# Kernel tuning notes

Hardware: AMD Instinct MI355X
Metric: run time of the kernel (lower is better)

Reference implementation:

```python
import jax, jax.numpy as jnp
import numpy as np

B = 65536
N_HOSTS = 16
N_FEATS = 48        # 3 * n_hosts
N_WINDOW = 3
N_LATENT = 10
GAT_IN = 3
GAT_OUT = 16
E = N_WINDOW + GAT_OUT  # 19, MHA embed dim
PROTO_DIM = 10


def setup_inputs() -> dict:
    key = jax.random.key(0)
    ks = jax.random.split(key, 20)
    def rn(k, shape, scale=0.1):
        return jax.random.normal(k, shape, dtype=jnp.float32) * scale
    return {
        "t": jax.random.normal(ks[0], (B, N_WINDOW, N_FEATS), dtype=jnp.float32),
        "s": jnp.zeros((1,), jnp.float32),  # unused by forward, kept for signature fidelity
        "h0": jax.random.normal(ks[1], (B, 1, N_WINDOW), dtype=jnp.float32),
        "gru_Wih": rn(ks[2], (3 * N_WINDOW, N_FEATS)),
        "gru_Whh": rn(ks[3], (3 * N_WINDOW, N_WINDOW)),
        "gru_bih": rn(ks[4], (3 * N_WINDOW,)),
        "gru_bhh": rn(ks[5], (3 * N_WINDOW,)),
        "gat_W": rn(ks[6], (GAT_IN, GAT_OUT)),
        "gat_al": rn(ks[7], (GAT_OUT,)),
        "gat_ar": rn(ks[8], (GAT_OUT,)),
        "mha_Win": rn(ks[9], (3 * E, E)),
        "mha_bin": rn(ks[10], (3 * E,)),
        "mha_Wout": rn(ks[11], (E, E)),
        "mha_bout": rn(ks[12], (E,)),
        "enc_W": rn(ks[13], (N_HOSTS * N_LATENT, N_WINDOW * E)),
        "enc_b": rn(ks[14], (N_HOSTS * N_LATENT,)),
        "anom_W": rn(ks[15], (2, N_LATENT)),
        "anom_b": rn(ks[16], (2,)),
        "proto_W": rn(ks[17], (PROTO_DIM, N_LATENT)),
        "proto_b": rn(ks[18], (PROTO_DIM,)),
    }


def _forward(t, s, h0, gru_Wih, gru_Whh, gru_bih, gru_bhh,
             gat_W, gat_al, gat_ar, mha_Win, mha_bin, mha_Wout, mha_bout,
             enc_W, enc_b, anom_W, anom_b, proto_W, proto_b):
    # ---- GRU (seq-first, batch B, hidden = n_window = 3) ----
    xs = jnp.swapaxes(t, 0, 1)  # (3, B, 48)
    h0_ = h0[:, 0, :]           # (B, 3)

    def gru_step(h, x_t):
        gi = x_t @ gru_Wih.T + gru_bih   # (B, 9)
        gh = h @ gru_Whh.T + gru_bhh     # (B, 9)
        i_r, i_z, i_n = jnp.split(gi, 3, axis=-1)
        h_r, h_z, h_n = jnp.split(gh, 3, axis=-1)
        r = jax.nn.sigmoid(i_r + h_r)
        z = jax.nn.sigmoid(i_z + h_z)
        n = jnp.tanh(i_n + r * h_n)
        h_new = (1.0 - z) * n + z * h
        return h_new, h_new

    _, gru_out = jax.lax.scan(gru_step, h0_, xs)  # (3, B, 3)

    # ---- GAT on fully-connected 16-node graph (with self loops) ----
    gin = t.reshape(t.shape[0], N_WINDOW, N_HOSTS, GAT_IN)      # (B, 3, 16, 3)
    z = jnp.einsum("bwnc,cf->bwnf", gin, gat_W)                 # (B, 3, 16, 16)
    el = z @ gat_al                                              # src scores (B,3,16)
    er = z @ gat_ar                                              # dst scores (B,3,16)
    e = jax.nn.leaky_relu(er[..., :, None] + el[..., None, :], 0.2)  # (B,3,v,u)
    alpha = jax.nn.softmax(e, axis=-1)                           # softmax over sources u
    gat_nodes = jnp.einsum("bwvu,bwuf->bwvf", alpha, z)          # (B, 3, 16, 16)
    gat_out = gat_nodes.mean(axis=2)                             # (B, 3, 16) mean over hosts
    gat_out = jnp.swapaxes(gat_out, 0, 1)                        # (3, B, 16)

    # ---- concat + single-head MHA (embed=19) ----
    c = jnp.concatenate([gru_out, gat_out], axis=-1)             # (3, B, 19)
    Wq, Wk, Wv = jnp.split(mha_Win, 3, axis=0)
    bq, bk, bv = jnp.split(mha_bin, 3, axis=0)
    q = c @ Wq.T + bq
    k = c @ Wk.T + bk
    v = c @ Wv.T + bv
    scores = jnp.einsum("sbe,tbe->bst", q, k) / jnp.sqrt(jnp.float32(E))
    attw = jax.nn.softmax(scores, axis=-1)
    attn = jnp.einsum("bst,tbe->sbe", attw, v)
    attn = attn @ mha_Wout.T + mha_bout                          # (3, B, 19)

    # ---- encoder: Linear(57,160); LeakyReLU(True) => negative_slope=1.0 => identity ----
    flat = jnp.swapaxes(attn, 0, 1).reshape(-1, N_WINDOW * E)    # (B, 57), seq-major flatten
    latent = flat @ enc_W.T + enc_b                              # (B, 160)
    latent = latent.reshape(-1, N_HOSTS, N_LATENT)               # (B, 16, 10)

    # ---- per-host tiny decoders, vectorized ----
    anomaly = jax.nn.softmax(latent @ anom_W.T + anom_b, axis=-1)   # (B, 16, 2)
    proto = jax.nn.sigmoid(latent @ proto_W.T + proto_b)            # (B, 16, PROTO_DIM)
    return anomaly, proto


def reference(t, s, h0, gru_Wih, gru_Whh, gru_bih, gru_bhh,
              gat_W, gat_al, gat_ar, mha_Win, mha_bin, mha_Wout, mha_bout,
              enc_W, enc_b, anom_W, anom_b, proto_W, proto_b):
    return _forward(t, s, h0, gru_Wih, gru_Whh, gru_bih, gru_bhh,
                    gat_W, gat_al, gat_ar, mha_Win, mha_bin, mha_Wout, mha_bout,
                    enc_W, enc_b, anom_W, anom_b, proto_W, proto_b)
```

## Files before the change

### kernel.cpp

```cpp
#include <hip/hip_runtime.h>

#define NW 3
#define NF 48
#define NHOST 16
#define NLAT 10
#define GOUT 16
#define EDIM 19
#define PDIM 10

#define CB_M    0
#define CB_P    361
#define CB_G    722
#define CB_H    741
#define CB_R    760
#define CB_C0   779
#define CB_WAL  780
#define CB_WAR  783
#define CB_CBIG 800
#define CB_BF   976
#define CB_TOT  10240

typedef __attribute__((ext_vector_type(8))) short bf16x8;
typedef __attribute__((ext_vector_type(4))) float f32x4;

__device__ __forceinline__ float frcp(float x){ return __builtin_amdgcn_rcpf(x); }
__device__ __forceinline__ float fsig(float x){ return frcp(1.f + __expf(-x)); }
__device__ __forceinline__ float ftanh(float x){ return 1.f - 2.f*frcp(1.f + __expf(2.f*x)); }
__device__ __forceinline__ unsigned short f2bf(float x){
    union { float f; unsigned u; } v; v.f = x;
    unsigned r = v.u + 0x7FFFu + ((v.u >> 16) & 1u);
    return (unsigned short)(r >> 16);
}
__device__ __forceinline__ float bf2f(unsigned short s){
    union { unsigned u; float f; } v; v.u = ((unsigned)s) << 16; return v.f;
}

__global__ __launch_bounds__(256) void k_const(
    const float* __restrict__ Win, const float* __restrict__ bin,
    const float* __restrict__ Wout, const float* __restrict__ bout,
    const float* __restrict__ gatW, const float* __restrict__ gal,
    const float* __restrict__ gar, const float* __restrict__ encW,
    const float* __restrict__ encb,
    const float* __restrict__ aW, const float* __restrict__ ab,
    const float* __restrict__ pW, const float* __restrict__ pb,
    float* __restrict__ cb)
{
    const int w = blockIdx.x*blockDim.x + threadIdx.x;
    if (w < 786) {
        const int idx = w;
        float acc = 0.f;
        if (idx < 361) {
            int i = idx/19, j = idx%19;
            for (int e = 0; e < EDIM; ++e) acc += Win[e*EDIM+i]*Win[(EDIM+e)*EDIM+j];
        } else if (idx < 722) {
            int k = idx-361; int i = k/19, j = k%19;
            for (int e = 0; e < EDIM; ++e) acc += Wout[i*EDIM+e]*Win[(2*EDIM+e)*EDIM+j];
        } else if (idx < 741) {
            int j = idx-722;
            for (int e = 0; e < EDIM; ++e) acc += bin[e]*Win[(EDIM+e)*EDIM+j];
        } else if (idx < 760) {
            int i = idx-741;
            for (int e = 0; e < EDIM; ++e) acc += Win[e*EDIM+i]*bin[EDIM+e];
        } else if (idx < 779) {
            int i = idx-760; acc = bout[i];
            for (int e = 0; e < EDIM; ++e) acc += Wout[i*EDIM+e]*bin[2*EDIM+e];
        } else if (idx == 779) {
            for (int e = 0; e < EDIM; ++e) acc += bin[e]*bin[EDIM+e];
        } else {
            int c = idx-780; int cc = c%3; bool left = c<3;
            for (int f2 = 0; f2 < GOUT; ++f2)
                acc += gatW[cc*GOUT+f2]*(left ? gal[f2] : gar[f2]);
        }
        cb[idx] = acc;
    } else if (w < 962) {
        const int g = w - 786;
        int host = g / 11, jj = g % 11;
        float acc = (jj == 0) ? (ab[0] - ab[1]) : pb[jj-1];
        for (int l = 0; l < NLAT; ++l) {
            float coef = (jj == 0) ? (aW[l] - aW[NLAT+l]) : pW[(jj-1)*NLAT + l];
            acc += coef * encb[host*NLAT + l];
        }
        cb[CB_CBIG + g] = acc;
    } else if (w < 12226) {
        unsigned short* bf = (unsigned short*)(cb + CB_BF);
        const int u = w - 962;
        int j    = u & 7;
        int lane = (u >> 3) & 63;
        int tile = u >> 9;
        int half = tile / 11, n = tile % 11;
        int k = half*32 + ((lane >> 4) & 3)*8 + j;
        int g = n*16 + (lane & 15);
        float acc = 0.f;
        if (k < 57) {
            int host = g / 11, jj = g % 11;
            for (int l = 0; l < NLAT; ++l) {
                float coef = (jj == 0) ? (aW[l] - aW[NLAT+l]) : pW[(jj-1)*NLAT + l];
                acc += coef * encW[(host*NLAT + l)*57 + k];
            }
        }
        bf[u] = f2bf(acc);
    }
}

__global__ __launch_bounds__(64, 4) void k_fused(
    const float* __restrict__ t, const float* __restrict__ h0,
    const float* __restrict__ Wih, const float* __restrict__ bih,
    const float* __restrict__ gatW, const float* __restrict__ Whh,
    const float* __restrict__ bhh, const float* __restrict__ cb,
    float* __restrict__ outA, float* __restrict__ outP, int B)
{
    __shared__ __align__(16) char smraw[9600];
    __shared__ __align__(16) unsigned short a2[16][64];
    float (*fm)[25][16]     = reinterpret_cast<float(*)[25][16]>(smraw);
    unsigned short (*xs)[50]= reinterpret_cast<unsigned short(*)[50]>(smraw + 4800);
    float (*mtb)[EDIM][16]  = reinterpret_cast<float(*)[EDIM][16]>(smraw + 4800);
    float (*pcb)[EDIM][16]  = reinterpret_cast<float(*)[EDIM][16]>(smraw + 4800);
    float (*gtb)[16]        = reinterpret_cast<float(*)[16]>(smraw + 4800 + 3648);
    _Float16 (*lg)[178]     = reinterpret_cast<_Float16(*)[178]>(smraw);

    const int lane = threadIdx.x;
    const int b0   = blockIdx.x * 16;
    const int bl   = lane & 15;
    const int sw   = lane >> 4;

    if (lane < 48) {
        const int w = sw;
        const float* tp = t + ((size_t)(b0 + bl)*NW + w)*NF;
        unsigned short* xrow = xs[lane];

        const float Wal0=cb[CB_WAL],Wal1=cb[CB_WAL+1],Wal2=cb[CB_WAL+2];
        const float War0=cb[CB_WAR],War1=cb[CB_WAR+1],War2=cb[CB_WAR+2];

        float gi[9];
#pragma unroll
        for (int r = 0; r < 9; ++r) gi[r] = bih[r];
        float el[NHOST], er[NHOST];
#pragma unroll
        for (int c = 0; c < 4; ++c) {
            float xc[12];
#pragma unroll
            for (int i = 0; i < 3; ++i) {
                float4 v = *reinterpret_cast<const float4*>(tp + c*12 + i*4);
                xc[i*4+0]=v.x; xc[i*4+1]=v.y; xc[i*4+2]=v.z; xc[i*4+3]=v.w;
            }
#pragma unroll
            for (int k = 0; k < 12; ++k) xrow[c*12 + k] = f2bf(xc[k]);
#pragma unroll
            for (int r = 0; r < 9; ++r) {
                float a = 0.f;
#pragma unroll
                for (int k = 0; k < 12; ++k) a += xc[k]*Wih[r*NF + c*12 + k];
                gi[r] += a;
            }
#pragma unroll
            for (int u = 0; u < 4; ++u) {
                const int uu = c*4 + u;
                el[uu] = xc[u*3]*Wal0 + xc[u*3+1]*Wal1 + xc[u*3+2]*Wal2;
                er[uu] = xc[u*3]*War0 + xc[u*3+1]*War1 + xc[u*3+2]*War2;
            }
        }
#pragma unroll
        for (int r = 0; r < 9; ++r) fm[w][r][bl] = gi[r];

        float beta[NHOST];
#pragma unroll
        for (int u = 0; u < NHOST; ++u) beta[u] = 0.f;
#pragma unroll
        for (int v = 0; v < NHOST; ++v) {
            float ee[NHOST]; float sum = 0.f;
#pragma unroll
            for (int u = 0; u < NHOST; ++u) {
                float s = er[v] + el[u];
                s = fmaxf(s, 0.2f*s);
                ee[u] = __expf(s); sum += ee[u];
            }
            float inv = frcp(sum);
#pragma unroll
            for (int u = 0; u < NHOST; ++u) beta[u] += ee[u]*inv;
        }
        float g0=0.f, g1=0.f, g2=0.f;
#pragma unroll
        for (int u = 0; u < NHOST; ++u) {
            float bu = beta[u]*(1.f/16.f);
            g0 += bu*bf2f(xrow[u*3+0]);
            g1 += bu*bf2f(xrow[u*3+1]);
            g2 += bu*bf2f(xrow[u*3+2]);
        }
#pragma unroll
        for (int f2 = 0; f2 < GOUT; ++f2)
            fm[w][9+f2][bl] = g0*gatW[f2] + g1*gatW[GOUT+f2] + g2*gatW[2*GOUT+f2];
    }
    __syncthreads();

    float cw[EDIM];
    float hsv = 0.f, aw0 = 0.f, aw1 = 0.f, aw2 = 0.f;
#pragma unroll
    for (int i = 0; i < EDIM; ++i) cw[i] = 0.f;

    if (lane < 48) {
        const int s = sw;
        const int b = b0 + bl;
        float h[3] = { h0[(size_t)b*3+0], h0[(size_t)b*3+1], h0[(size_t)b*3+2] };
        float ch[NW][3];
#pragma unroll
        for (int w = 0; w < NW; ++w) {
            float gi[9];
#pragma unroll
            for (int r = 0; r < 9; ++r) gi[r] = fm[w][r][bl];
            float gh[9];
#pragma unroll
            for (int r = 0; r < 9; ++r)
                gh[r] = bhh[r] + h[0]*Whh[r*3+0] + h[1]*Whh[r*3+1] + h[2]*Whh[r*3+2];
#pragma unroll
            for (int j = 0; j < 3; ++j) {
                float rg = fsig(gi[j]   + gh[j]);
                float zg = fsig(gi[3+j] + gh[3+j]);
                float ng = ftanh(gi[6+j] + rg*gh[6+j]);
                h[j] = (1.f - zg)*ng + zg*h[j];
            }
            ch[w][0]=h[0]; ch[w][1]=h[1]; ch[w][2]=h[2];
        }
#pragma unroll
        for (int j = 0; j < 3; ++j)
            cw[j] = (s==0) ? ch[0][j] : (s==1) ? ch[1][j] : ch[2][j];
#pragma unroll
        for (int f2 = 0; f2 < GOUT; ++f2)
            cw[3+f2] = fm[s][9+f2][bl];
    }
    __syncthreads();

    if (lane < 48) {
        const int s = sw;
        float gt = 0.f;
#pragma unroll
        for (int i = 0; i < EDIM; ++i) { hsv += cw[i]*cb[CB_H+i]; gt += cw[i]*cb[CB_G+i]; }
#pragma unroll
        for (int i = 0; i < EDIM; ++i) {
            float a = 0.f;
#pragma unroll
            for (int j = 0; j < EDIM; ++j) a += cb[CB_M+i*EDIM+j]*cw[j];
            mtb[s][i][bl] = a;
        }
        gtb[s][bl] = gt;
    }
    __syncthreads();

    if (lane < 48) {
        const float c0 = cb[CB_C0];
        float sc[NW];
#pragma unroll
        for (int tt = 0; tt < NW; ++tt) {
            float a = 0.f;
#pragma unroll
            for (int i = 0; i < EDIM; ++i) a += cw[i]*mtb[tt][i][bl];
            sc[tt] = (a + gtb[tt][bl] + hsv + c0) * 0.2294157338705618f;
        }
        float m = fmaxf(sc[0], fmaxf(sc[1], sc[2]));
        float e0=__expf(sc[0]-m), e1=__expf(sc[1]-m), e2=__expf(sc[2]-m);
        float inv = frcp(e0+e1+e2);
        aw0=e0*inv; aw1=e1*inv; aw2=e2*inv;
    }
    __syncthreads();

    if (lane < 48) {
        const int s = sw;
#pragma unroll
        for (int i = 0; i < EDIM; ++i) {
            float a = 0.f;
#pragma unroll
            for (int j = 0; j < EDIM; ++j) a += cb[CB_P+i*EDIM+j]*cw[j];
            pcb[s][i][bl] = a;
        }
    }
    __syncthreads();

    if (lane < 48) {
        const int s = sw;
        char* a2c = (char*)a2;
        const int swz = (bl & 7) << 4;
#pragma unroll
        for (int i = 0; i < EDIM; ++i) {
            float v = cb[CB_R+i] + aw0*pcb[0][i][bl] + aw1*pcb[1][i][bl]
                    + aw2*pcb[2][i][bl];
            const int byte = bl*128 + (s*EDIM + i)*2;
            *reinterpret_cast<unsigned short*>(a2c + (byte ^ swz)) = f2bf(v);
        }
        if (s == 0) {
#pragma unroll
            for (int r = 0; r < 7; ++r) {
                const int byte = bl*128 + (57 + r)*2;
                *reinterpret_cast<unsigned short*>(a2c + (byte ^ swz)) = 0;
            }
        }
    }
    __syncthreads();

    {
        const int browl = lane & 15;
        const int koff  = (lane >> 4) * 8;
        const char* a2c = (const char*)a2;
        const int swz = (browl & 7) << 4;
        union { uint4 q; bf16x8 v; } a0, a1;
        a0.q = *reinterpret_cast<const uint4*>(a2c + ((browl*128 + koff*2) ^ swz));
        a1.q = *reinterpret_cast<const uint4*>(a2c + ((browl*128 + 64 + koff*2) ^ swz));

        const uint4* bfq = (const uint4*)(cb + CB_BF);
        const int r0 = (lane >> 4) << 2;
#pragma unroll
        for (int n = 0; n < 11; ++n) {
            union { uint4 q; bf16x8 v; } bf0, bf1;
            bf0.q = bfq[(size_t)n*64 + lane];
            bf1.q = bfq[(size_t)(11 + n)*64 + lane];
            f32x4 acc = {0.f, 0.f, 0.f, 0.f};
            acc = __builtin_amdgcn_mfma_f32_16x16x32_bf16(a0.v, bf0.v, acc, 0, 0, 0);
            acc = __builtin_amdgcn_mfma_f32_16x16x32_bf16(a1.v, bf1.v, acc, 0, 0, 0);
            const int c = n*16 + (lane & 15);
#pragma unroll
            for (int r = 0; r < 4; ++r) lg[r0 + r][c] = (_Float16)acc[r];
        }
    }
    __syncthreads();

    {
        const int host = lane & 15;
        const int tg   = lane >> 4;
        const float* cbig = cb + CB_CBIG;
#pragma unroll
        for (int i = 0; i < 4; ++i) {
            const int bll = tg + 4*i;
            const int b   = b0 + bll;
            float v[11];
#pragma unroll
            for (int jj = 0; jj < 11; ++jj)
                v[jj] = (float)lg[bll][host*11 + jj] + cbig[host*11 + jj];
            float p0 = fsig(v[0]);
            float2 av; av.x = p0; av.y = 1.f - p0;
            *reinterpret_cast<float2*>(outA + (size_t)b*32 + host*2) = av;
            float* pP = outP + (size_t)b*160 + host*10;
#pragma unroll
            for (int p = 0; p < 5; ++p) {
                float2 pv; pv.x = fsig(v[1 + 2*p]); pv.y = fsig(v[2 + 2*p]);
                *reinterpret_cast<float2*>(pP + 2*p) = pv;
            }
        }
    }
}

extern "C" void kernel_launch(void* const* d_in, const int* in_sizes, int n_in,
                              void* d_out, int out_size, void* d_ws, size_t ws_size,
                              hipStream_t stream) {
    const float* t    = (const float*)d_in[0];
    const float* h0   = (const float*)d_in[2];
    const float* Wih  = (const float*)d_in[3];
    const float* Whh  = (const float*)d_in[4];
    const float* bih  = (const float*)d_in[5];
    const float* bhh  = (const float*)d_in[6];
    const float* gatW = (const float*)d_in[7];
    const float* gal  = (const float*)d_in[8];
    const float* gar  = (const float*)d_in[9];
    const float* Win  = (const float*)d_in[10];
    const float* bin  = (const float*)d_in[11];
    const float* Wout = (const float*)d_in[12];
    const float* bout = (const float*)d_in[13];
    const float* encW = (const float*)d_in[14];
    const float* encb = (const float*)d_in[15];
    const float* aW   = (const float*)d_in[16];
    const float* ab   = (const float*)d_in[17];
    const float* pW   = (const float*)d_in[18];
    const float* pb   = (const float*)d_in[19];

    const int B = in_sizes[0] / (NW * NF);
    float* cb  = (float*)d_ws;
    float* outA = (float*)d_out;
    float* outP = (float*)d_out + (size_t)B*32;

    k_const<<<dim3(48), 256, 0, stream>>>(Win, bin, Wout, bout, gatW, gal, gar,
                                          encW, encb, aW, ab, pW, pb, cb);
    k_fused<<<dim3(B/16), 64, 0, stream>>>(t, h0, Wih, bih, gatW, Whh, bhh, cb,
                                           outA, outP, B);
}
```

Baseline: 66.18 us.

## Stage input tile into LDS with coalesced loads and merge sync phases

All 64 lanes now cooperatively load the block's 16-sample input tile with contiguous float4 reads into an fp32 shared buffer. Previously each of 48 threads issued strided float4 loads and stored a bf16 copy. The GAT aggregation now reads fp32 values instead of bf16-rounded ones. The pcb buffer gets its own shared region so the mtb, score and pcb phases can be merged, which removes two __syncthreads. Shared memory per block grows, which may lower occupancy.

```diff
diff --git a/kernel.cpp b/kernel.cpp
--- a/kernel.cpp
+++ b/kernel.cpp
@@ -30,9 +30,6 @@
     union { float f; unsigned u; } v; v.f = x;
     unsigned r = v.u + 0x7FFFu + ((v.u >> 16) & 1u);
     return (unsigned short)(r >> 16);
-}
-__device__ __forceinline__ float bf2f(unsigned short s){
-    union { unsigned u; float f; } v; v.u = ((unsigned)s) << 16; return v.f;
 }
 
 __global__ __launch_bounds__(256) void k_const(
@@ -109,24 +106,36 @@
     const float* __restrict__ bhh, const float* __restrict__ cb,
     float* __restrict__ outA, float* __restrict__ outP, int B)
 {
-    __shared__ __align__(16) char smraw[9600];
+    __shared__ __align__(16) char smraw[14784];
     __shared__ __align__(16) unsigned short a2[16][64];
-    float (*fm)[25][16]     = reinterpret_cast<float(*)[25][16]>(smraw);
-    unsigned short (*xs)[50]= reinterpret_cast<unsigned short(*)[50]>(smraw + 4800);
-    float (*mtb)[EDIM][16]  = reinterpret_cast<float(*)[EDIM][16]>(smraw + 4800);
-    float (*pcb)[EDIM][16]  = reinterpret_cast<float(*)[EDIM][16]>(smraw + 4800);
-    float (*gtb)[16]        = reinterpret_cast<float(*)[16]>(smraw + 4800 + 3648);
-    _Float16 (*lg)[178]     = reinterpret_cast<_Float16(*)[178]>(smraw);
+    float (*fm)[25][16]    = reinterpret_cast<float(*)[25][16]>(smraw);
+    float (*xs2)[52]       = reinterpret_cast<float(*)[52]>(smraw + 4800);
+    float (*mtb)[EDIM][16] = reinterpret_cast<float(*)[EDIM][16]>(smraw + 4800);
+    float (*gtb)[16]       = reinterpret_cast<float(*)[16]>(smraw + 4800 + 3648);
+    float (*pcb)[EDIM][16] = reinterpret_cast<float(*)[EDIM][16]>(smraw + 4800 + 3840);
+    _Float16 (*lg)[178]    = reinterpret_cast<_Float16(*)[178]>(smraw);
 
     const int lane = threadIdx.x;
     const int b0   = blockIdx.x * 16;
     const int bl   = lane & 15;
     const int sw   = lane >> 4;
 
+    {
+        const float4* tq = reinterpret_cast<const float4*>(t + (size_t)b0*NW*NF);
+#pragma unroll
+        for (int r = 0; r < 9; ++r) {
+            const int f = lane + 64*r;
+            float4 v = tq[f];
+            const int b_   = f / 36;
+            const int off4 = f - b_*36;
+            const int w_   = off4 / 12, j4 = off4 - w_*12;
+            *reinterpret_cast<float4*>(&xs2[b_*3 + w_][j4*4]) = v;
+        }
+    }
+    __syncthreads();
+
     if (lane < 48) {
-        const int w = sw;
-        const float* tp = t + ((size_t)(b0 + bl)*NW + w)*NF;
-        unsigned short* xrow = xs[lane];
+        const float* xrow = xs2[bl*3 + sw];
 
         const float Wal0=cb[CB_WAL],Wal1=cb[CB_WAL+1],Wal2=cb[CB_WAL+2];
         const float War0=cb[CB_WAR],War1=cb[CB_WAR+1],War2=cb[CB_WAR+2];
@@ -139,12 +148,7 @@
         for (int c = 0; c < 4; ++c) {
             float xc[12];
 #pragma unroll
-            for (int i = 0; i < 3; ++i) {
-                float4 v = *reinterpret_cast<const float4*>(tp + c*12 + i*4);
-                xc[i*4+0]=v.x; xc[i*4+1]=v.y; xc[i*4+2]=v.z; xc[i*4+3]=v.w;
-            }
-#pragma unroll
-            for (int k = 0; k < 12; ++k) xrow[c*12 + k] = f2bf(xc[k]);
+            for (int k = 0; k < 12; ++k) xc[k] = xrow[c*12 + k];
 #pragma unroll
             for (int r = 0; r < 9; ++r) {
                 float a = 0.f;
@@ -159,6 +163,7 @@
                 er[uu] = xc[u*3]*War0 + xc[u*3+1]*War1 + xc[u*3+2]*War2;
             }
         }
+        const int w = sw;
 #pragma unroll
         for (int r = 0; r < 9; ++r) fm[w][r][bl] = gi[r];
 
@@ -182,9 +187,7 @@
 #pragma unroll
         for (int u = 0; u < NHOST; ++u) {
             float bu = beta[u]*(1.f/16.f);
-            g0 += bu*bf2f(xrow[u*3+0]);
-            g1 += bu*bf2f(xrow[u*3+1]);
-            g2 += bu*bf2f(xrow[u*3+2]);
+            g0 += bu*xrow[u*3+0]; g1 += bu*xrow[u*3+1]; g2 += bu*xrow[u*3+2];
         }
 #pragma unroll
         for (int f2 = 0; f2 < GOUT; ++f2)
@@ -226,26 +229,23 @@
 #pragma unroll
         for (int f2 = 0; f2 < GOUT; ++f2)
             cw[3+f2] = fm[s][9+f2][bl];
+
+        float gt = 0.f;
+#pragma unroll
+        for (int i = 0; i < EDIM; ++i) { hsv += cw[i]*cb[CB_H+i]; gt += cw[i]*cb[CB_G+i]; }
+#pragma unroll
+        for (int i = 0; i < EDIM; ++i) {
+            float a = 0.f;
+#pragma unroll
+            for (int j = 0; j < EDIM; ++j) a += cb[CB_M+i*EDIM+j]*cw[j];
+            mtb[s][i][bl] = a;
+        }
+        gtb[s][bl] = gt;
     }
     __syncthreads();
 
     if (lane < 48) {
         const int s = sw;
-        float gt = 0.f;
-#pragma unroll
-        for (int i = 0; i < EDIM; ++i) { hsv += cw[i]*cb[CB_H+i]; gt += cw[i]*cb[CB_G+i]; }
-#pragma unroll
-        for (int i = 0; i < EDIM; ++i) {
-            float a = 0.f;
-#pragma unroll
-            for (int j = 0; j < EDIM; ++j) a += cb[CB_M+i*EDIM+j]*cw[j];
-            mtb[s][i][bl] = a;
-        }
-        gtb[s][bl] = gt;
-    }
-    __syncthreads();
-
-    if (lane < 48) {
         const float c0 = cb[CB_C0];
         float sc[NW];
 #pragma unroll
@@ -259,11 +259,7 @@
         float e0=__expf(sc[0]-m), e1=__expf(sc[1]-m), e2=__expf(sc[2]-m);
         float inv = frcp(e0+e1+e2);
         aw0=e0*inv; aw1=e1*inv; aw2=e2*inv;
-    }
-    __syncthreads();
-
-    if (lane < 48) {
-        const int s = sw;
+
 #pragma unroll
         for (int i = 0; i < EDIM; ++i) {
             float a = 0.f;
```

Result: slower. 69.80 us (+5.5%).
